# Optimization experiments

Hardware: AMD Instinct MI355X
Metric: run time of the kernel (lower is better)

The kernel has to match this reference:

```python
import jax, jax.numpy as jnp
import numpy as np

N = 50000
E = 600000
C = 128


def setup_inputs() -> dict:
    key = jax.random.key(0)
    ks = jax.random.split(key, 16)
    s = 0.05
    return {
        "x": jax.random.normal(ks[0], (N, C), dtype=jnp.float32),
        "pos": jax.random.normal(ks[1], (N, 3), dtype=jnp.float32),
        "edge_index": jax.random.randint(ks[2], (2, E), 0, N, dtype=jnp.int64),
        # mlp_h: Linear(C,C) -> ReLU -> Linear(C,3) -> Tanh
        "h_w1": jax.random.normal(ks[3], (C, C), dtype=jnp.float32) * s,
        "h_b1": jnp.zeros((C,), dtype=jnp.float32),
        "h_w2": jax.random.normal(ks[4], (C, 3), dtype=jnp.float32) * s,
        "h_b2": jnp.zeros((3,), dtype=jnp.float32),
        # mlp_f: Linear(C+3,C) -> ReLU
        "f_w": jax.random.normal(ks[5], (C + 3, C), dtype=jnp.float32) * s,
        "f_b": jnp.zeros((C,), dtype=jnp.float32),
        # mlp_g: Linear(C,C) -> ReLU -> Linear(C,C)
        "g_w1": jax.random.normal(ks[6], (C, C), dtype=jnp.float32) * s,
        "g_b1": jnp.zeros((C,), dtype=jnp.float32),
        "g_w2": jax.random.normal(ks[7], (C, C), dtype=jnp.float32) * s,
        "g_b2": jnp.zeros((C,), dtype=jnp.float32),
    }


def reference(x, pos, edge_index, h_w1, h_b1, h_w2, h_b2, f_w, f_b,
              g_w1, g_b1, g_w2, g_b2):
    src = edge_index[0]  # j (source)
    dst = edge_index[1]  # i (target)
    # per-node predicted offset: delta_i = mlp_h(x_i)  [N,3]
    delta = jnp.tanh(jax.nn.relu(x @ h_w1 + h_b1) @ h_w2 + h_b2)
    # per-edge message: mlp_f(cat(pos_j - pos_i + delta_i, x_j))  [E,C]
    e = jnp.concatenate([pos[src] - pos[dst] + delta[dst], x[src]], axis=-1)
    m = jax.nn.relu(e @ f_w + f_b)
    # scatter-sum to target nodes  [N,C]
    aggr = jax.ops.segment_sum(m, dst, num_segments=x.shape[0])
    # node update + residual
    out = jax.nn.relu(aggr @ g_w1 + g_b1) @ g_w2 + g_b2
    return x + out
```

## Files before the change

### kernel.cpp

```cpp
#include <hip/hip_runtime.h>
#include <cstdint>
#include <cstddef>

#define TPB 256
#define PTPB 1024
#define QTPB 512
#define LPAD 136
#define CAP 48
#define CSTRIDE 64

using frag_ab = __attribute__((ext_vector_type(8))) short;
using f32x4   = __attribute__((ext_vector_type(4))) float;
using u16x4   = __attribute__((ext_vector_type(4))) ushort;

__device__ inline ushort f2b(float f) {
    uint u = __builtin_bit_cast(uint, f);
    u = (u + 0x7FFFu + ((u >> 16) & 1u)) >> 16;
    return (ushort)u;
}
__device__ inline float b2f_lo(uint u) { return __builtin_bit_cast(float, u << 16); }
__device__ inline float b2f_hi(uint u) { return __builtin_bit_cast(float, u & 0xFFFF0000u); }

__global__ __launch_bounds__(TPB) void pack_kernel(
    const float* __restrict__ h_w1, const float* __restrict__ f_w,
    const float* __restrict__ g_w1, const float* __restrict__ g_w2,
    short* __restrict__ W1pk, short* __restrict__ Wfpk,
    short* __restrict__ G1pk, short* __restrict__ G2pk,
    int* __restrict__ deg, int M)
{
    int m   = blockIdx.y;
    int fid = blockIdx.x * TPB + threadIdx.x;
    int lane = fid & 63, ks = (fid >> 6) & 3, nt = fid >> 8;
    const float* src; short* dst; int rowoff = 0;
    if      (m == 0) { src = h_w1; dst = W1pk; }
    else if (m == 1) { src = f_w;  dst = Wfpk; rowoff = 3; }
    else if (m == 2) { src = g_w1; dst = G1pk; }
    else             { src = g_w2; dst = G2pk; }
    int col   = nt * 16 + (lane & 15);
    int kbase = ks * 32 + ((lane >> 4) << 3);
    frag_ab f;
#pragma unroll
    for (int j = 0; j < 8; ++j)
        f[j] = (short)f2b(src[(size_t)(rowoff + kbase + j) * 128 + col]);
    *(frag_ab*)(dst + (((size_t)(nt * 4 + ks) * 64 + lane) << 3)) = f;

    int flat = (blockIdx.y * gridDim.x + blockIdx.x) * TPB + threadIdx.x;
    int nthr = gridDim.y * gridDim.x * TPB;
    for (int i = flat; i < M; i += nthr) deg[i] = 0;
}

__global__ __launch_bounds__(PTPB) void prehist_kernel(
    const float* __restrict__ x, const float* __restrict__ pos,
    const short* __restrict__ W1pk,
    const float* __restrict__ h_b1,
    const float* __restrict__ h_w2, const float* __restrict__ h_b2,
    const float* __restrict__ f_w, const float* __restrict__ f_b,
    ushort* __restrict__ A2h, ushort* __restrict__ Bvh,
    const int* __restrict__ ei, int* __restrict__ deg,
    ushort* __restrict__ sspad, int M, int E, int echunk)
{
    __shared__ short wlds[32768];
    const int tid  = threadIdx.x;
    const int lane = tid & 63;
    const int wave = tid >> 6;
    const int kg   = lane >> 4;
    const int node = blockIdx.x * 256 + wave * 16 + (lane & 15);
    const int nc   = node < M ? node : M - 1;

    float4 xv0[4], xv1[4];
#pragma unroll
    for (int ks = 0; ks < 4; ++ks) {
        const float* px = x + (size_t)nc * 128 + ks * 32 + kg * 8;
        xv0[ks] = *(const float4*)px;
        xv1[ks] = *(const float4*)(px + 4);
    }
    float p0 = pos[(size_t)nc * 3 + 0];
    float p1 = pos[(size_t)nc * 3 + 1];
    float p2 = pos[(size_t)nc * 3 + 2];

    const int base = blockIdx.x * echunk;
    int end = base + echunk; if (end > E) end = E;
    int esrc[3], edst[3];
    bool ev[3];
#pragma unroll
    for (int t = 0; t < 3; ++t) {
        int i = base + tid + t * PTPB;
        ev[t] = (i < end);
        int ic = ev[t] ? i : base;
        esrc[t] = ei[ic];
        edst[t] = ei[E + ic];
    }

#pragma unroll
    for (int i = 0; i < 4; ++i) {
        int id = i * PTPB + tid;
        *(int4*)(wlds + (size_t)id * 8) = *(const int4*)(W1pk + (size_t)id * 8);
    }

    frag_ab xb[4];
#pragma unroll
    for (int ks = 0; ks < 4; ++ks) {
        frag_ab f;
        f[0] = (short)f2b(xv0[ks].x); f[1] = (short)f2b(xv0[ks].y);
        f[2] = (short)f2b(xv0[ks].z); f[3] = (short)f2b(xv0[ks].w);
        f[4] = (short)f2b(xv1[ks].x); f[5] = (short)f2b(xv1[ks].y);
        f[6] = (short)f2b(xv1[ks].z); f[7] = (short)f2b(xv1[ks].w);
        xb[ks] = f;
    }
    __syncthreads();

    f32x4 acch[8], acca[8];
#pragma unroll
    for (int nt = 0; nt < 8; ++nt) { acch[nt] = (f32x4)0.f; acca[nt] = (f32x4)0.f; }
#pragma unroll
    for (int ks = 0; ks < 4; ++ks) {
#pragma unroll
        for (int nt = 0; nt < 8; ++nt) {
            frag_ab wh = *(const frag_ab*)(wlds + (((nt * 4 + ks) * 64 + lane) << 3));
            acch[nt] = __builtin_amdgcn_mfma_f32_16x16x32_bf16(wh, xb[ks], acch[nt], 0, 0, 0);
            frag_ab wf = *(const frag_ab*)(wlds + 16384 + (((nt * 4 + ks) * 64 + lane) << 3));
            acca[nt] = __builtin_amdgcn_mfma_f32_16x16x32_bf16(wf, xb[ks], acca[nt], 0, 0, 0);
        }
    }

    float d0 = 0.f, d1 = 0.f, d2 = 0.f;
#pragma unroll
    for (int nt = 0; nt < 8; ++nt) {
        int f0 = nt * 16 + kg * 4;
        float4 b1 = *(const float4*)(h_b1 + f0);
        float w2[12];
        *(float4*)(w2 + 0) = *(const float4*)(h_w2 + f0 * 3);
        *(float4*)(w2 + 4) = *(const float4*)(h_w2 + f0 * 3 + 4);
        *(float4*)(w2 + 8) = *(const float4*)(h_w2 + f0 * 3 + 8);
#pragma unroll
        for (int j = 0; j < 4; ++j) {
            float h = fmaxf(acch[nt][j] + ((const float*)&b1)[j], 0.f);
            d0 += h * w2[j * 3 + 0];
            d1 += h * w2[j * 3 + 1];
            d2 += h * w2[j * 3 + 2];
        }
    }
    d0 += __shfl_xor(d0, 16); d0 += __shfl_xor(d0, 32);
    d1 += __shfl_xor(d1, 16); d1 += __shfl_xor(d1, 32);
    d2 += __shfl_xor(d2, 16); d2 += __shfl_xor(d2, 32);
    d0 = tanhf(d0 + h_b2[0]);
    d1 = tanhf(d1 + h_b2[1]);
    d2 = tanhf(d2 + h_b2[2]);

    if (node < M) {
#pragma unroll
        for (int nt = 0; nt < 8; ++nt) {
            int f0 = nt * 16 + kg * 4;
            float4 w0 = *(const float4*)(f_w + f0);
            float4 w1 = *(const float4*)(f_w + 128 + f0);
            float4 w2 = *(const float4*)(f_w + 256 + f0);
            float4 fb = *(const float4*)(f_b + f0);
            u16x4 av, bv;
#pragma unroll
            for (int j = 0; j < 4; ++j) {
                float ww0 = ((const float*)&w0)[j];
                float ww1 = ((const float*)&w1)[j];
                float ww2 = ((const float*)&w2)[j];
                float pw = p0 * ww0 + p1 * ww1 + p2 * ww2;
                float dw = d0 * ww0 + d1 * ww1 + d2 * ww2;
                av[j] = f2b(acca[nt][j] + pw);
                bv[j] = f2b(((const float*)&fb)[j] + dw - pw);
            }
            *(u16x4*)(A2h + (size_t)node * 128 + f0) = av;
            *(u16x4*)(Bvh + (size_t)node * 128 + f0) = bv;
        }
    }

#pragma unroll
    for (int t = 0; t < 3; ++t) {
        if (ev[t]) {
            int p = atomicAdd(&deg[edst[t]], 1);
            if (p < CAP) sspad[edst[t] * CSTRIDE + p] = (ushort)esrc[t];
        }
    }
}

__global__ __launch_bounds__(TPB) void reduce_kernel(
    const int* __restrict__ deg, const ushort* __restrict__ sspad,
    const ushort* __restrict__ A2h, const ushort* __restrict__ Bvh,
    ushort* __restrict__ aggr, int M)
{
    int row = blockIdx.x * 4 + (threadIdx.x >> 6);
    if (row >= M) return;
    int lane = threadIdx.x & 63;
    int half = lane >> 5;
    int cl   = (lane & 31) * 4;

    uint2 bu = *(const uint2*)(Bvh + (size_t)row * 128 + cl);
    float b0 = b2f_lo(bu.x), b1 = b2f_hi(bu.x);
    float b2 = b2f_lo(bu.y), b3 = b2f_hi(bu.y);
    float a0 = 0.f, a1 = 0.f, a2 = 0.f, a3 = 0.f;

    const ushort* bkt = sspad + (size_t)row * CSTRIDE;
    int k1 = deg[row]; if (k1 > CAP) k1 = CAP;
    int k  = half;
    for (; k + 2 < k1; k += 4) {
        int s0 = bkt[k], s1 = bkt[k + 2];
        uint2 u0 = *(const uint2*)(A2h + (size_t)s0 * 128 + cl);
        uint2 u1 = *(const uint2*)(A2h + (size_t)s1 * 128 + cl);
        a0 += fmaxf(b2f_lo(u0.x) + b0, 0.f) + fmaxf(b2f_lo(u1.x) + b0, 0.f);
        a1 += fmaxf(b2f_hi(u0.x) + b1, 0.f) + fmaxf(b2f_hi(u1.x) + b1, 0.f);
        a2 += fmaxf(b2f_lo(u0.y) + b2, 0.f) + fmaxf(b2f_lo(u1.y) + b2, 0.f);
        a3 += fmaxf(b2f_hi(u0.y) + b3, 0.f) + fmaxf(b2f_hi(u1.y) + b3, 0.f);
    }
    for (; k < k1; k += 2) {
        uint2 u0 = *(const uint2*)(A2h + (size_t)bkt[k] * 128 + cl);
        a0 += fmaxf(b2f_lo(u0.x) + b0, 0.f);
        a1 += fmaxf(b2f_hi(u0.x) + b1, 0.f);
        a2 += fmaxf(b2f_lo(u0.y) + b2, 0.f);
        a3 += fmaxf(b2f_hi(u0.y) + b3, 0.f);
    }
    a0 += __shfl_xor(a0, 32);
    a1 += __shfl_xor(a1, 32);
    a2 += __shfl_xor(a2, 32);
    a3 += __shfl_xor(a3, 32);

    if (half == 0) {
        uint2 r;
        r.x = (uint)f2b(a0) | ((uint)f2b(a1) << 16);
        r.y = (uint)f2b(a2) | ((uint)f2b(a3) << 16);
        *(uint2*)(aggr + (size_t)row * 128 + cl) = r;
    }
}

__global__ __launch_bounds__(QTPB) void post_kernel(
    const float* __restrict__ x, const ushort* __restrict__ aggr,
    const short* __restrict__ G1pk, const float* __restrict__ g_b1,
    const short* __restrict__ G2pk, const float* __restrict__ g_b2,
    float* __restrict__ out, int M)
{
    __shared__ short glds[16384];
    __shared__ short bounce[8 * 16 * LPAD];
    const int tid  = threadIdx.x;
    const int lane = tid & 63;
    const int wave = tid >> 6;
    const int kg   = lane >> 4;
    short* ws = bounce + wave * 16 * LPAD;

    const int node = blockIdx.x * 128 + wave * 16 + (lane & 15);
    const int nc   = node < M ? node : M - 1;

    frag_ab ab[4];
#pragma unroll
    for (int ks = 0; ks < 4; ++ks)
        ab[ks] = *(const frag_ab*)(aggr + (size_t)nc * 128 + ks * 32 + kg * 8);

#pragma unroll
    for (int i = 0; i < 4; ++i) {
        int id = i * QTPB + tid;
        *(int4*)(glds + (size_t)id * 8) = *(const int4*)(G1pk + (size_t)id * 8);
    }
    __syncthreads();

    f32x4 h2[8];
#pragma unroll
    for (int nt = 0; nt < 8; ++nt) h2[nt] = (f32x4)0.f;
#pragma unroll
    for (int ks = 0; ks < 4; ++ks) {
#pragma unroll
        for (int nt = 0; nt < 8; ++nt) {
            frag_ab g = *(const frag_ab*)(glds + (((nt * 4 + ks) * 64 + lane) << 3));
            h2[nt] = __builtin_amdgcn_mfma_f32_16x16x32_bf16(g, ab[ks], h2[nt], 0, 0, 0);
        }
    }
#pragma unroll
    for (int nt = 0; nt < 8; ++nt) {
        int f0 = nt * 16 + kg * 4;
        float4 gb = *(const float4*)(g_b1 + f0);
        u16x4 hv;
#pragma unroll
        for (int j = 0; j < 4; ++j)
            hv[j] = f2b(fmaxf(h2[nt][j] + ((const float*)&gb)[j], 0.f));
        *(u16x4*)(ws + (lane & 15) * LPAD + f0) = hv;
    }
    __syncthreads();

#pragma unroll
    for (int i = 0; i < 4; ++i) {
        int id = i * QTPB + tid;
        *(int4*)(glds + (size_t)id * 8) = *(const int4*)(G2pk + (size_t)id * 8);
    }
    __syncthreads();

    f32x4 o[8];
#pragma unroll
    for (int nt = 0; nt < 8; ++nt) o[nt] = (f32x4)0.f;
#pragma unroll
    for (int ks = 0; ks < 4; ++ks) {
        frag_ab bfr = *(const frag_ab*)(ws + (lane & 15) * LPAD + ks * 32 + kg * 8);
#pragma unroll
        for (int nt = 0; nt < 8; ++nt) {
            frag_ab g = *(const frag_ab*)(glds + (((nt * 4 + ks) * 64 + lane) << 3));
            o[nt] = __builtin_amdgcn_mfma_f32_16x16x32_bf16(g, bfr, o[nt], 0, 0, 0);
        }
    }

    __syncthreads();
    float* ob = (float*)glds + (wave << 10);
    const int nhalf = (lane & 15) >> 3;
#pragma unroll
    for (int p = 0; p < 2; ++p) {
        if (nhalf == p) {
            int ln = lane & 7;
#pragma unroll
            for (int nt = 0; nt < 8; ++nt) {
                float4 v;
                v.x = o[nt][0]; v.y = o[nt][1]; v.z = o[nt][2]; v.w = o[nt][3];
                *(float4*)(ob + ln * 128 + nt * 16 + kg * 4) = v;
            }
        }
#pragma unroll
        for (int it = 0; it < 4; ++it) {
            int ln2 = lane >> 3;
            int cc  = (lane & 7) + it * 8;
            float4 v = *(const float4*)(ob + ln2 * 128 + cc * 4);
            int gn = blockIdx.x * 128 + wave * 16 + p * 8 + ln2;
            if (gn < M) {
                float4 xv = *(const float4*)(x + (size_t)gn * 128 + cc * 4);
                float4 gb = *(const float4*)(g_b2 + cc * 4);
                float4 ov;
                ov.x = v.x + gb.x + xv.x; ov.y = v.y + gb.y + xv.y;
                ov.z = v.z + gb.z + xv.z; ov.w = v.w + gb.w + xv.w;
                *(float4*)(out + (size_t)gn * 128 + cc * 4) = ov;
            }
        }
    }
}

extern "C" void kernel_launch(void* const* d_in, const int* in_sizes, int n_in,
                              void* d_out, int out_size, void* d_ws, size_t ws_size,
                              hipStream_t stream)
{
    const float* x    = (const float*)d_in[0];
    const float* pos  = (const float*)d_in[1];
    const int*   ei   = (const int*)d_in[2];
    const float* h_w1 = (const float*)d_in[3];
    const float* h_b1 = (const float*)d_in[4];
    const float* h_w2 = (const float*)d_in[5];
    const float* h_b2 = (const float*)d_in[6];
    const float* f_w  = (const float*)d_in[7];
    const float* f_b  = (const float*)d_in[8];
    const float* g_w1 = (const float*)d_in[9];
    const float* g_b1 = (const float*)d_in[10];
    const float* g_w2 = (const float*)d_in[11];
    const float* g_b2 = (const float*)d_in[12];

    const int M = in_sizes[1] / 3;
    const int E = in_sizes[2] / 2;
    const int nbp = (M + 255) / 256;
    const int nbq = (M + 127) / 128;
    const int echunk = (E + nbp - 1) / nbp;

    ushort* A2h  = (ushort*)d_ws;
    ushort* Bvh  = A2h + (size_t)M * 128;
    ushort* aggr = Bvh + (size_t)M * 128;
    short* W1pk  = (short*)(aggr + (size_t)M * 128);
    short* Wfpk  = W1pk + 16384;
    short* G1pk  = Wfpk + 16384;
    short* G2pk  = G1pk + 16384;
    int* deg     = (int*)(G2pk + 16384);
    ushort* sspad = (ushort*)(deg + M);
    float* out   = (float*)d_out;

    pack_kernel<<<dim3(8, 4), TPB, 0, stream>>>(h_w1, f_w, g_w1, g_w2,
                                                W1pk, Wfpk, G1pk, G2pk,
                                                deg, M);
    prehist_kernel<<<nbp, PTPB, 0, stream>>>(x, pos, W1pk, h_b1, h_w2, h_b2,
                                             f_w, f_b, A2h, Bvh,
                                             ei, deg, sspad, M, E, echunk);
    reduce_kernel<<<(M + 3) / 4, TPB, 0, stream>>>(deg, sspad, A2h, Bvh, aggr, M);
    post_kernel<<<nbq, QTPB, 0, stream>>>(x, aggr, G1pk, g_b1, G2pk, g_b2, out, M);
}
```

Measured before the change: 96.27 us.

## Shrink prehist blocks to 256 threads and stage two weight matrices sequentially

The node-preprocessing kernel now runs 256-thread blocks covering 64 nodes instead of 1024-thread blocks covering 256 nodes. The two packed weight matrices are loaded into shared memory one after the other, with barriers between them, so LDS use is halved. Only one set of eight MFMA accumulators is live at a time instead of two. The aim is lower register and LDS pressure, higher occupancy and finer-grained scheduling, at the cost of four times as many per-block weight reloads from L2 and extra barriers.

```diff
diff --git a/kernel.cpp b/kernel.cpp
--- a/kernel.cpp
+++ b/kernel.cpp
@@ -3,7 +3,6 @@
 #include <cstddef>
 
 #define TPB 256
-#define PTPB 1024
 #define QTPB 512
 #define LPAD 136
 #define CAP 48
@@ -49,7 +48,7 @@
     for (int i = flat; i < M; i += nthr) deg[i] = 0;
 }
 
-__global__ __launch_bounds__(PTPB) void prehist_kernel(
+__global__ __launch_bounds__(TPB) void prehist_kernel(
     const float* __restrict__ x, const float* __restrict__ pos,
     const short* __restrict__ W1pk,
     const float* __restrict__ h_b1,
@@ -59,12 +58,12 @@
     const int* __restrict__ ei, int* __restrict__ deg,
     ushort* __restrict__ sspad, int M, int E, int echunk)
 {
-    __shared__ short wlds[32768];
+    __shared__ short wlds[16384];
     const int tid  = threadIdx.x;
     const int lane = tid & 63;
     const int wave = tid >> 6;
     const int kg   = lane >> 4;
-    const int node = blockIdx.x * 256 + wave * 16 + (lane & 15);
+    const int node = blockIdx.x * 64 + wave * 16 + (lane & 15);
     const int nc   = node < M ? node : M - 1;
 
     float4 xv0[4], xv1[4];
@@ -84,7 +83,7 @@
     bool ev[3];
 #pragma unroll
     for (int t = 0; t < 3; ++t) {
-        int i = base + tid + t * PTPB;
+        int i = base + tid + t * TPB;
         ev[t] = (i < end);
         int ic = ev[t] ? i : base;
         esrc[t] = ei[ic];
@@ -92,8 +91,8 @@
     }
 
 #pragma unroll
-    for (int i = 0; i < 4; ++i) {
-        int id = i * PTPB + tid;
+    for (int i = 0; i < 8; ++i) {
+        int id = i * TPB + tid;
         *(int4*)(wlds + (size_t)id * 8) = *(const int4*)(W1pk + (size_t)id * 8);
     }
 
@@ -109,18 +108,23 @@
     }
     __syncthreads();
 
-    f32x4 acch[8], acca[8];
-#pragma unroll
-    for (int nt = 0; nt < 8; ++nt) { acch[nt] = (f32x4)0.f; acca[nt] = (f32x4)0.f; }
-#pragma unroll
-    for (int ks = 0; ks < 4; ++ks) {
+    f32x4 acch[8];
+#pragma unroll
+    for (int nt = 0; nt < 8; ++nt) acch[nt] = (f32x4)0.f;
+#pragma unroll
+    for (int ks = 0; ks < 4; ++ks)
 #pragma unroll
         for (int nt = 0; nt < 8; ++nt) {
             frag_ab wh = *(const frag_ab*)(wlds + (((nt * 4 + ks) * 64 + lane) << 3));
             acch[nt] = __builtin_amdgcn_mfma_f32_16x16x32_bf16(wh, xb[ks], acch[nt], 0, 0, 0);
-            frag_ab wf = *(const frag_ab*)(wlds + 16384 + (((nt * 4 + ks) * 64 + lane) << 3));
-            acca[nt] = __builtin_amdgcn_mfma_f32_16x16x32_bf16(wf, xb[ks], acca[nt], 0, 0, 0);
-        }
+        }
+    __syncthreads();
+
+#pragma unroll
+    for (int i = 0; i < 8; ++i) {
+        int id = i * TPB + tid;
+        *(int4*)(wlds + (size_t)id * 8) =
+            *(const int4*)(W1pk + 16384 + (size_t)id * 8);
     }
 
     float d0 = 0.f, d1 = 0.f, d2 = 0.f;
@@ -146,6 +150,18 @@
     d0 = tanhf(d0 + h_b2[0]);
     d1 = tanhf(d1 + h_b2[1]);
     d2 = tanhf(d2 + h_b2[2]);
+    __syncthreads();
+
+    f32x4 acca[8];
+#pragma unroll
+    for (int nt = 0; nt < 8; ++nt) acca[nt] = (f32x4)0.f;
+#pragma unroll
+    for (int ks = 0; ks < 4; ++ks)
+#pragma unroll
+        for (int nt = 0; nt < 8; ++nt) {
+            frag_ab wf = *(const frag_ab*)(wlds + (((nt * 4 + ks) * 64 + lane) << 3));
+            acca[nt] = __builtin_amdgcn_mfma_f32_16x16x32_bf16(wf, xb[ks], acca[nt], 0, 0, 0);
+        }
 
     if (node < M) {
 #pragma unroll
@@ -352,7 +368,7 @@
 
     const int M = in_sizes[1] / 3;
     const int E = in_sizes[2] / 2;
-    const int nbp = (M + 255) / 256;
+    const int nbp = (M + 63) / 64;
     const int nbq = (M + 127) / 128;
     const int echunk = (E + nbp - 1) / nbp;
 
@@ -370,9 +386,9 @@
     pack_kernel<<<dim3(8, 4), TPB, 0, stream>>>(h_w1, f_w, g_w1, g_w2,
                                                 W1pk, Wfpk, G1pk, G2pk,
                                                 deg, M);
-    prehist_kernel<<<nbp, PTPB, 0, stream>>>(x, pos, W1pk, h_b1, h_w2, h_b2,
-                                             f_w, f_b, A2h, Bvh,
-                                             ei, deg, sspad, M, E, echunk);
+    prehist_kernel<<<nbp, TPB, 0, stream>>>(x, pos, W1pk, h_b1, h_w2, h_b2,
+                                            f_w, f_b, A2h, Bvh,
+                                            ei, deg, sspad, M, E, echunk);
     reduce_kernel<<<(M + 3) / 4, TPB, 0, stream>>>(deg, sspad, A2h, Bvh, aggr, M);
     post_kernel<<<nbq, QTPB, 0, stream>>>(x, aggr, G1pk, g_b1, G2pk, g_b2, out, M);
 }
```

Result: slower. 124.6 us (+29.4%).
